# Kernel optimization log

Hardware: AMD Instinct MI355X
Metric: run time of the kernel (lower is better)

The kernel has to match this reference:

```python
import jax, jax.numpy as jnp
import numpy as np

B = 16384
MV = 512   # movie_vector_size
UV = 512   # user_vector_size
NM = 16    # num_dense_movie_embeddings
NU = 16    # num_dense_user_embeddings
DS = 16    # dense_embedding_size
MLP = [256, 128, 1]


def setup_inputs() -> dict:
    key = jax.random.key(0)
    ks = jax.random.split(key, 12)
    inp = {
        'movie_vectors': jax.random.normal(ks[0], (B, MV), jnp.float32),
        'user_vectors': jax.random.normal(ks[1], (B, UV), jnp.float32),
        # embedding towers: Linear(in, DS*N + 1), stored as [in, out]
        'Wm': jax.random.normal(ks[2], (MV, DS * NM + 1), jnp.float32) * (1.0 / np.sqrt(MV)),
        'bm': jax.random.normal(ks[3], (DS * NM + 1,), jnp.float32) * 0.01,
        'Wu': jax.random.normal(ks[4], (UV, DS * NU + 1), jnp.float32) * (1.0 / np.sqrt(UV)),
        'bu': jax.random.normal(ks[5], (DS * NU + 1,), jnp.float32) * 0.01,
    }
    d_in = (NM + NU) * DS  # 512
    dims = [d_in] + MLP
    for i in range(len(MLP)):
        inp[f'W{i+1}'] = jax.random.normal(ks[6 + 2*i], (dims[i], dims[i+1]), jnp.float32) * (1.0 / np.sqrt(dims[i]))
        inp[f'b{i+1}'] = jax.random.normal(ks[7 + 2*i], (dims[i+1],), jnp.float32) * 0.01
    return inp


def reference(movie_vectors, user_vectors, Wm, bm, Wu, bu, W1, b1, W2, b2, W3, b3):
    batch = movie_vectors.shape[0]
    movie_dense = movie_vectors @ Wm + bm          # [B, DS*NM+1]
    user_dense = user_vectors @ Wu + bu            # [B, DS*NU+1]
    fm_additive = movie_dense[:, -1] + user_dense[:, -1]            # [B]
    m_split = movie_dense[:, :-1].reshape(batch, NM, DS)            # [B, NM, DS]
    u_split = user_dense[:, :-1].reshape(batch, NU, DS)             # [B, NU, DS]
    fm_interactions = jnp.einsum('bik,bjk->bij', m_split, u_split).reshape(batch, -1)  # [B, NM*NU]
    all_dense = jnp.concatenate([movie_dense[:, :-1], user_dense[:, :-1]], axis=-1)    # [B, (NM+NU)*DS]
    h = jax.nn.relu(all_dense @ W1 + b1)
    h = jax.nn.relu(h @ W2 + b2)
    mlp_out = h @ W3 + b3                                           # [B, 1]
    logit = mlp_out + fm_additive[:, None] + jnp.sum(fm_interactions, axis=-1, keepdims=True)
    return logit
```

## Files before the change

### kernel.cpp

```cpp
#include <hip/hip_runtime.h>


#define NTH 1024
#define RB  64

typedef __bf16 bf16x8 __attribute__((ext_vector_type(8)));
typedef float  f32x4  __attribute__((ext_vector_type(4)));

#define WS_WMF  0
#define WS_WUF  294912
#define WS_W1F  589824
#define WS_W2F  851968
#define WS_BIAS 917504

#define BPITCH  528
#define L_BST   0
#define L_DENSE 67584
#define L_FM    133120
#define L_ADD   141824
#define L_OUT   142336
#define LDSB    142592

__device__ __forceinline__ unsigned short f2bf(float f) {
  unsigned u = __builtin_bit_cast(unsigned, f);
  u += 0x7FFFu + ((u >> 16) & 1u);
  return (unsigned short)(u >> 16);
}

__device__ __forceinline__ unsigned cvtpk(float a, float b) {
  unsigned r;
  asm("v_cvt_pk_bf16_f32 %0, %1, %2" : "=v"(r) : "v"(a), "v"(b));
  return r;
}

__device__ __forceinline__ f32x4 mfma_bf16(bf16x8 a, bf16x8 b, f32x4 c) {
  return __builtin_amdgcn_mfma_f32_16x16x32_bf16(a, b, c, 0, 0, 0);
}

extern "C" __global__ __launch_bounds__(256) void deepfm_prep(
    const float* __restrict__ Wm, const float* __restrict__ bm,
    const float* __restrict__ Wu, const float* __restrict__ bu,
    const float* __restrict__ W1, const float* __restrict__ W2,
    const float* __restrict__ b3, char* __restrict__ ws) {
  const int unit = blockIdx.x * 4 + (threadIdx.x >> 6);
  if (unit >= 897) return;
  const int l = threadIdx.x & 63;
  const int fi = l & 15, q = l >> 4;
  unsigned short h[8];
  if (unit < 576) {
    const int t = unit / 288, rem = unit % 288;
    const int kg = rem / 18, ft = rem % 18;
    const float* W = t ? Wu : Wm;
    char* outp = ws + (t ? WS_WUF : WS_WMF);
    const int f = ft * 16 + fi;
#pragma unroll
    for (int e = 0; e < 8; ++e) {
      const int k = kg * 32 + q * 8 + e;
      float val;
      if (f < 256) val = W[k * 257 + f];
      else if (f < 272) {
        float s = 0.f;
#pragma unroll
        for (int i = 0; i < 16; ++i) s += W[k * 257 + i * 16 + (f - 256)];
        val = s;
      } else if (f == 272) val = W[k * 257 + 256];
      else val = 0.f;
      h[e] = f2bf(val);
    }
    uint4 o;
    o.x = h[0] | ((unsigned)h[1] << 16); o.y = h[2] | ((unsigned)h[3] << 16);
    o.z = h[4] | ((unsigned)h[5] << 16); o.w = h[6] | ((unsigned)h[7] << 16);
    *(uint4*)(outp + (((kg * 18 + ft) * 64 + l) << 4)) = o;
  } else if (unit < 832) {
    const int bb = unit - 576;
    const int kg = bb / 16, ft = bb % 16;
    const int f = ft * 16 + fi;
#pragma unroll
    for (int e = 0; e < 8; ++e) h[e] = f2bf(W1[(kg * 32 + q * 8 + e) * 256 + f]);
    uint4 o;
    o.x = h[0] | ((unsigned)h[1] << 16); o.y = h[2] | ((unsigned)h[3] << 16);
    o.z = h[4] | ((unsigned)h[5] << 16); o.w = h[6] | ((unsigned)h[7] << 16);
    *(uint4*)(ws + WS_W1F + (((kg * 16 + ft) * 64 + l) << 4)) = o;
  } else if (unit < 896) {
    const int bb = unit - 832;
    const int kg = bb / 8, ft = bb % 8;
    const int f = ft * 16 + fi;
#pragma unroll
    for (int e = 0; e < 8; ++e) h[e] = f2bf(W2[(kg * 32 + q * 8 + e) * 128 + f]);
    uint4 o;
    o.x = h[0] | ((unsigned)h[1] << 16); o.y = h[2] | ((unsigned)h[3] << 16);
    o.z = h[4] | ((unsigned)h[5] << 16); o.w = h[6] | ((unsigned)h[7] << 16);
    *(uint4*)(ws + WS_W2F + (((kg * 8 + ft) * 64 + l) << 4)) = o;
  } else {
    float* aux = (float*)(ws + WS_BIAS);
    if (l < 16) {
      float s = 0.f;
      for (int i = 0; i < 16; ++i) s += bm[i * 16 + l];
      aux[l] = s;
    } else if (l < 32) {
      const int k = l - 16;
      float s = 0.f;
      for (int i = 0; i < 16; ++i) s += bu[i * 16 + k];
      aux[l] = s;
    } else if (l == 32) {
      aux[32] = bm[256] + bu[256] + b3[0];
    }
  }
}

extern "C" __global__ __launch_bounds__(NTH)
__attribute__((amdgpu_waves_per_eu(4, 4))) void deepfm_main(
    const float* __restrict__ movie, const float* __restrict__ user,
    const float* __restrict__ bm, const float* __restrict__ bu,
    const float* __restrict__ b1, const float* __restrict__ b2,
    const float* __restrict__ W3, const char* __restrict__ ws,
    float* __restrict__ out) {
  extern __shared__ __align__(16) char lds[];
  char* const bstage    = lds + L_BST;
  char* const densefrag = lds + L_DENSE;
  char* const h1frag    = lds + L_BST;
  float* const fmbuf    = (float*)(lds + L_FM);
  float* const addbuf   = (float*)(lds + L_ADD);
  float* const outpart  = (float*)(lds + L_OUT);

  const int tid = threadIdx.x;
  const int w   = tid >> 6;
  const int l   = tid & 63;
  const int cn  = l & 15;
  const int q   = l >> 4;
  const int row0 = blockIdx.x * RB;

  const int tw   = w >> 3;
  const int wi   = w & 7;
  const int axi  = wi & 1;
  const int rtb  = (wi >> 1) * 2;

  const int rot  = (int)blockIdx.x >> 3;
  const int hord = rot & 1;
  const int kk0  = (rot >> 1) & 7;
  const int p2r  = rot & 15;
  const int p3r  = rot & 7;

  const f32x4 zz = {0.f, 0.f, 0.f, 0.f};
  const float* auxb = (const float*)(ws + WS_BIAS);

  bf16x8 p2a, p2b;
  bf16x8 p3a, p3b;

  {
    const char* WF = ws + (tw ? WS_WUF : WS_WMF);
    const char* brow = bstage + tw * 64 * BPITCH;
    f32x4 a0r0 = zz, a0r1 = zz, a0r2 = zz, a0r3 = zz;
    f32x4 a1r0 = zz, a1r1 = zz, a1r2 = zz, a1r3 = zz;
    f32x4 axc0 = zz, axc1 = zz;

    const int h0 = hord, h1h = hord ^ 1;

#pragma unroll
    for (int p = 0; p < 8; ++p) {
      const int idx = p * 1024 + tid;
      const int rr = idx >> 6, f4 = idx & 63;
      const float* src = (rr >= 64) ? user : movie;
      const float4 v = *(const float4*)(src + (size_t)(row0 + (rr & 63)) * 512 +
                                        h0 * 256 + f4 * 4);
      uint2 o;
      o.x = cvtpk(v.x, v.y);
      o.y = cvtpk(v.z, v.w);
      *(uint2*)(bstage + rr * BPITCH + f4 * 8) = o;
    }
    __syncthreads();

    float4 pf[8];
#pragma unroll
    for (int p = 0; p < 8; ++p) {
      const int idx = p * 1024 + tid;
      const int rr = idx >> 6, f4 = idx & 63;
      const float* src = (rr >= 64) ? user : movie;
      pf[p] = *(const float4*)(src + (size_t)(row0 + (rr & 63)) * 512 +
                               h1h * 256 + f4 * 4);
    }
    uint2 pfc[8];

#pragma unroll
    for (int i = 0; i < 8; ++i) {
      const int kgl = (kk0 + i) & 7;
      const int kg  = h0 * 8 + kgl;
      const bf16x8 bf0 = *(const bf16x8*)(brow + cn * BPITCH + kgl * 64 + q * 16);
      const bf16x8 bf1 = *(const bf16x8*)(brow + (16 + cn) * BPITCH + kgl * 64 + q * 16);
      const bf16x8 bf2 = *(const bf16x8*)(brow + (32 + cn) * BPITCH + kgl * 64 + q * 16);
      const bf16x8 bf3 = *(const bf16x8*)(brow + (48 + cn) * BPITCH + kgl * 64 + q * 16);
      const bf16x8 A0 = *(const bf16x8*)(WF + (((kg * 18 + wi * 2 + 0) * 64 + l) << 4));
      const bf16x8 A1 = *(const bf16x8*)(WF + (((kg * 18 + wi * 2 + 1) * 64 + l) << 4));
      bf16x8 AX;
      if (wi < 4) AX = *(const bf16x8*)(WF + (((kg * 18 + 16 + axi) * 64 + l) << 4));
      __builtin_amdgcn_s_setprio(1);
      a0r0 = mfma_bf16(A0, bf0, a0r0);  a0r1 = mfma_bf16(A0, bf1, a0r1);
      a0r2 = mfma_bf16(A0, bf2, a0r2);  a0r3 = mfma_bf16(A0, bf3, a0r3);
      a1r0 = mfma_bf16(A1, bf0, a1r0);  a1r1 = mfma_bf16(A1, bf1, a1r1);
      a1r2 = mfma_bf16(A1, bf2, a1r2);  a1r3 = mfma_bf16(A1, bf3, a1r3);
      if (wi < 4) {
        const bf16x8 bs0 = rtb ? bf2 : bf0;
        const bf16x8 bs1 = rtb ? bf3 : bf1;
        axc0 = mfma_bf16(AX, bs0, axc0);
        axc1 = mfma_bf16(AX, bs1, axc1);
      }
      __builtin_amdgcn_s_setprio(0);
      if (i >= 1) {
        const int j = i - 1;
        pfc[j].x = cvtpk(pf[j].x, pf[j].y);
        pfc[j].y = cvtpk(pf[j].z, pf[j].w);
      }
    }
    pfc[7].x = cvtpk(pf[7].x, pf[7].y);
    pfc[7].y = cvtpk(pf[7].z, pf[7].w);

    __syncthreads();

    bf16x8 A0c = *(const bf16x8*)(WF + ((((h1h * 8 + kk0) * 18 + wi * 2 + 0) * 64 + l) << 4));
    bf16x8 A1c = *(const bf16x8*)(WF + ((((h1h * 8 + kk0) * 18 + wi * 2 + 1) * 64 + l) << 4));

#pragma unroll
    for (int p = 0; p < 8; ++p) {
      const int idx = p * 1024 + tid;
      const int rr = idx >> 6, f4 = idx & 63;
      *(uint2*)(bstage + rr * BPITCH + f4 * 8) = pfc[p];
    }
    __syncthreads();

#pragma unroll
    for (int i = 0; i < 8; ++i) {
      const int kgl = (kk0 + i) & 7;
      const int kg  = h1h * 8 + kgl;
      const bf16x8 bf0 = *(const bf16x8*)(brow + cn * BPITCH + kgl * 64 + q * 16);
      const bf16x8 bf1 = *(const bf16x8*)(brow + (16 + cn) * BPITCH + kgl * 64 + q * 16);
      const bf16x8 bf2 = *(const bf16x8*)(brow + (32 + cn) * BPITCH + kgl * 64 + q * 16);
      const bf16x8 bf3 = *(const bf16x8*)(brow + (48 + cn) * BPITCH + kgl * 64 + q * 16);
      bf16x8 AX;
      if (wi < 4) AX = *(const bf16x8*)(WF + (((kg * 18 + 16 + axi) * 64 + l) << 4));
      bf16x8 A0n, A1n;
      if (i < 7) {
        const int nkg = h1h * 8 + ((kk0 + i + 1) & 7);
        A0n = *(const bf16x8*)(WF + (((nkg * 18 + wi * 2 + 0) * 64 + l) << 4));
        A1n = *(const bf16x8*)(WF + (((nkg * 18 + wi * 2 + 1) * 64 + l) << 4));
      } else {
        A0n = A0c; A1n = A1c;
      }
      __builtin_amdgcn_s_setprio(1);
      a0r0 = mfma_bf16(A0c, bf0, a0r0);  a0r1 = mfma_bf16(A0c, bf1, a0r1);
      a0r2 = mfma_bf16(A0c, bf2, a0r2);  a0r3 = mfma_bf16(A0c, bf3, a0r3);
      a1r0 = mfma_bf16(A1c, bf0, a1r0);  a1r1 = mfma_bf16(A1c, bf1, a1r1);
      a1r2 = mfma_bf16(A1c, bf2, a1r2);  a1r3 = mfma_bf16(A1c, bf3, a1r3);
      if (wi < 4) {
        const bf16x8 bs0 = rtb ? bf2 : bf0;
        const bf16x8 bs1 = rtb ? bf3 : bf1;
        axc0 = mfma_bf16(AX, bs0, axc0);
        axc1 = mfma_bf16(AX, bs1, axc1);
      }
      __builtin_amdgcn_s_setprio(0);
      A0c = A0n; A1c = A1n;
    }

    p2a = *(const bf16x8*)(ws + WS_W1F + (((p2r * 16 + w) * 64 + l) << 4));
    p2b = *(const bf16x8*)(ws + WS_W1F + (((((p2r + 1) & 15) * 16 + w) * 64 + l) << 4));

    const float* bt = tw ? bu : bm;
    const f32x4 accA[2][4] = {{a0r0, a0r1, a0r2, a0r3}, {a1r0, a1r1, a1r2, a1r3}};
#pragma unroll
    for (int s = 0; s < 2; ++s) {
      const int ft = wi * 2 + s;
      const int fb = ft * 16 + q * 4;
      const float g0 = bt[fb], g1 = bt[fb + 1], g2 = bt[fb + 2], g3 = bt[fb + 3];
      const int kd = tw * 256 + fb;
      const int kgd = kd >> 5, qd = (kd >> 3) & 3, ed = kd & 4;
#pragma unroll
      for (int rt = 0; rt < 4; ++rt) {
        const f32x4 v = accA[s][rt];
        uint2 p;
        p.x = cvtpk(v[0] + g0, v[1] + g1);
        p.y = cvtpk(v[2] + g2, v[3] + g3);
        *(uint2*)(densefrag + (((kgd * 4 + rt) * 64 + qd * 16 + cn) << 4) +
                  (ed ? 8 : 0)) = p;
      }
    }

    if (wi < 4) {
      if (axi == 0) {
#pragma unroll
        for (int reg = 0; reg < 4; ++reg) {
          fmbuf[(tw * 64 + rtb * 16 + cn) * 17 + (q * 4 + reg)] = axc0[reg];
          fmbuf[(tw * 64 + (rtb + 1) * 16 + cn) * 17 + (q * 4 + reg)] = axc1[reg];
        }
      } else if (q == 0) {
        addbuf[tw * 64 + rtb * 16 + cn] = axc0[0];
        addbuf[tw * 64 + (rtb + 1) * 16 + cn] = axc1[0];
      }
    }
  }

  __syncthreads();

  if (tid < 64) {
    float p = 0.f;
#pragma unroll
    for (int k = 0; k < 16; ++k)
      p += (fmbuf[tid * 17 + k] + auxb[k]) *
           (fmbuf[(64 + tid) * 17 + k] + auxb[16 + k]);
    outpart[tid] = p + addbuf[tid] + addbuf[64 + tid] + auxb[32];
  }

  {
    const char* W1F = ws + WS_W1F;
    bf16x8 a0c = p2a;
    bf16x8 a0n = p2b;
    f32x4 r0 = zz, r1 = zz, r2 = zz, r3 = zz;
#pragma unroll
    for (int i = 0; i < 16; ++i) {
      const int kg = (p2r + i) & 15;
      const bf16x8 b0 = *(const bf16x8*)(densefrag + (((kg * 4 + 0) * 64 + l) << 4));
      const bf16x8 b1f = *(const bf16x8*)(densefrag + (((kg * 4 + 1) * 64 + l) << 4));
      const bf16x8 b2f = *(const bf16x8*)(densefrag + (((kg * 4 + 2) * 64 + l) << 4));
      const bf16x8 b3f = *(const bf16x8*)(densefrag + (((kg * 4 + 3) * 64 + l) << 4));
      bf16x8 a2;
      if (i < 14) {
        const int nkg = (p2r + i + 2) & 15;
        a2 = *(const bf16x8*)(W1F + (((nkg * 16 + w) * 64 + l) << 4));
      }
      __builtin_amdgcn_s_setprio(1);
      r0 = mfma_bf16(a0c, b0,  r0);
      r1 = mfma_bf16(a0c, b1f, r1);
      r2 = mfma_bf16(a0c, b2f, r2);
      r3 = mfma_bf16(a0c, b3f, r3);
      __builtin_amdgcn_s_setprio(0);
      a0c = a0n;
      if (i < 14) a0n = a2;
    }

    if (w < 8) {
      p3a = *(const bf16x8*)(ws + WS_W2F + (((p3r * 8 + w) * 64 + l) << 4));
      p3b = *(const bf16x8*)(ws + WS_W2F + (((((p3r + 1) & 7) * 8 + w) * 64 + l) << 4));
    }

    const f32x4 accA[4] = {r0, r1, r2, r3};
    const int fb = w * 16 + q * 4;
    const float g0 = b1[fb], g1 = b1[fb + 1], g2 = b1[fb + 2], g3 = b1[fb + 3];
    const int kgd = fb >> 5, qd = (fb >> 3) & 3, ed = fb & 4;
#pragma unroll
    for (int rt = 0; rt < 4; ++rt) {
      const f32x4 v = accA[rt];
      uint2 p;
      p.x = cvtpk(fmaxf(v[0] + g0, 0.f), fmaxf(v[1] + g1, 0.f));
      p.y = cvtpk(fmaxf(v[2] + g2, 0.f), fmaxf(v[3] + g3, 0.f));
      *(uint2*)(h1frag + (((kgd * 4 + rt) * 64 + qd * 16 + cn) << 4) +
                (ed ? 8 : 0)) = p;
    }
  }

  __syncthreads();

  if (w < 8) {
    const char* W2F = ws + WS_W2F;
    bf16x8 a0c = p3a;
    bf16x8 a0n = p3b;
    f32x4 d0 = zz, d1 = zz, d2 = zz, d3 = zz;
#pragma unroll
    for (int i = 0; i < 8; ++i) {
      const int kg = (p3r + i) & 7;
      const bf16x8 b0 = *(const bf16x8*)(h1frag + (((kg * 4 + 0) * 64 + l) << 4));
      const bf16x8 b1f = *(const bf16x8*)(h1frag + (((kg * 4 + 1) * 64 + l) << 4));
      const bf16x8 b2f = *(const bf16x8*)(h1frag + (((kg * 4 + 2) * 64 + l) << 4));
      const bf16x8 b3f = *(const bf16x8*)(h1frag + (((kg * 4 + 3) * 64 + l) << 4));
      bf16x8 a2;
      if (i < 6) {
        const int nkg = (p3r + i + 2) & 7;
        a2 = *(const bf16x8*)(W2F + (((nkg * 8 + w) * 64 + l) << 4));
      }
      d0 = mfma_bf16(a0c, b0,  d0);
      d1 = mfma_bf16(a0c, b1f, d1);
      d2 = mfma_bf16(a0c, b2f, d2);
      d3 = mfma_bf16(a0c, b3f, d3);
      a0c = a0n;
      if (i < 6) a0n = a2;
    }
    const int fb = w * 16 + q * 4;
    float bb[4], ww[4];
#pragma unroll
    for (int i = 0; i < 4; ++i) { bb[i] = b2[fb + i]; ww[i] = W3[fb + i]; }
    const f32x4 acc3[4] = {d0, d1, d2, d3};
#pragma unroll
    for (int j = 0; j < 4; ++j) {
      float p = 0.f;
#pragma unroll
      for (int reg = 0; reg < 4; ++reg)
        p += fmaxf(acc3[j][reg] + bb[reg], 0.f) * ww[reg];
      p += __shfl_xor(p, 16, 64);
      p += __shfl_xor(p, 32, 64);
      if (l < 16) atomicAdd(&outpart[j * 16 + cn], p);
    }
  }

  __syncthreads();
  if (tid < 64) out[row0 + tid] = outpart[tid];
}

extern "C" void kernel_launch(void* const* d_in, const int* in_sizes, int n_in,
                              void* d_out, int out_size, void* d_ws, size_t ws_size,
                              hipStream_t stream) {
  const float* movie = (const float*)d_in[0];
  const float* user  = (const float*)d_in[1];
  const float* Wm = (const float*)d_in[2];
  const float* bm = (const float*)d_in[3];
  const float* Wu = (const float*)d_in[4];
  const float* bu = (const float*)d_in[5];
  const float* W1 = (const float*)d_in[6];
  const float* b1 = (const float*)d_in[7];
  const float* W2 = (const float*)d_in[8];
  const float* b2 = (const float*)d_in[9];
  const float* W3 = (const float*)d_in[10];
  const float* b3 = (const float*)d_in[11];
  char* ws = (char*)d_ws;
  float* out = (float*)d_out;

  (void)hipFuncSetAttribute((const void*)deepfm_main,
                            hipFuncAttributeMaxDynamicSharedMemorySize, LDSB);

  deepfm_prep<<<225, 256, 0, stream>>>(Wm, bm, Wu, bu, W1, W2, b3, ws);
  deepfm_main<<<256, NTH, LDSB, stream>>>(movie, user, bm, bu, b1, b2, W3, ws, out);
}
```

Before: 129.5 us.

## Halve rows per block to 32 with 512 threads, doubling grid size

Result: no change. 132.0 us (+1.9%).

```diff
diff --git a/kernel.cpp b/kernel.cpp
--- a/kernel.cpp
+++ b/kernel.cpp
@@ -1,8 +1,9 @@
 #include <hip/hip_runtime.h>
 
 
-#define NTH 1024
-#define RB  64
+#define NTH 512
+#define RB  32
+#define NBLK 512
 
 typedef __bf16 bf16x8 __attribute__((ext_vector_type(8)));
 typedef float  f32x4  __attribute__((ext_vector_type(4)));
@@ -15,11 +16,11 @@
 
 #define BPITCH  528
 #define L_BST   0
-#define L_DENSE 67584
-#define L_FM    133120
-#define L_ADD   141824
-#define L_OUT   142336
-#define LDSB    142592
+#define L_DENSE 33792
+#define L_FM    66560
+#define L_ADD   70912
+#define L_OUT   71168
+#define LDSB    71296
 
 __device__ __forceinline__ unsigned short f2bf(float f) {
   unsigned u = __builtin_bit_cast(unsigned, f);
@@ -130,10 +131,10 @@
   const int q   = l >> 4;
   const int row0 = blockIdx.x * RB;
 
-  const int tw   = w >> 3;
-  const int wi   = w & 7;
+  const int tw   = w >> 2;
+  const int wi   = w & 3;
   const int axi  = wi & 1;
-  const int rtb  = (wi >> 1) * 2;
+  const int axrt = wi >> 1;
 
   const int rot  = (int)blockIdx.x >> 3;
   const int hord = rot & 1;
@@ -149,19 +150,18 @@
 
   {
     const char* WF = ws + (tw ? WS_WUF : WS_WMF);
-    const char* brow = bstage + tw * 64 * BPITCH;
-    f32x4 a0r0 = zz, a0r1 = zz, a0r2 = zz, a0r3 = zz;
-    f32x4 a1r0 = zz, a1r1 = zz, a1r2 = zz, a1r3 = zz;
-    f32x4 axc0 = zz, axc1 = zz;
+    const char* brow = bstage + tw * 32 * BPITCH;
+    f32x4 ar[4][2] = {{zz, zz}, {zz, zz}, {zz, zz}, {zz, zz}};
+    f32x4 axc = zz;
 
     const int h0 = hord, h1h = hord ^ 1;
 
 #pragma unroll
     for (int p = 0; p < 8; ++p) {
-      const int idx = p * 1024 + tid;
+      const int idx = p * NTH + tid;
       const int rr = idx >> 6, f4 = idx & 63;
-      const float* src = (rr >= 64) ? user : movie;
-      const float4 v = *(const float4*)(src + (size_t)(row0 + (rr & 63)) * 512 +
+      const float* src = (rr >= 32) ? user : movie;
+      const float4 v = *(const float4*)(src + (size_t)(row0 + (rr & 31)) * 512 +
                                         h0 * 256 + f4 * 4);
       uint2 o;
       o.x = cvtpk(v.x, v.y);
@@ -173,10 +173,10 @@
     float4 pf[8];
 #pragma unroll
     for (int p = 0; p < 8; ++p) {
-      const int idx = p * 1024 + tid;
+      const int idx = p * NTH + tid;
       const int rr = idx >> 6, f4 = idx & 63;
-      const float* src = (rr >= 64) ? user : movie;
-      pf[p] = *(const float4*)(src + (size_t)(row0 + (rr & 63)) * 512 +
+      const float* src = (rr >= 32) ? user : movie;
+      pf[p] = *(const float4*)(src + (size_t)(row0 + (rr & 31)) * 512 +
                                h1h * 256 + f4 * 4);
     }
     uint2 pfc[8];
@@ -187,23 +187,18 @@
       const int kg  = h0 * 8 + kgl;
       const bf16x8 bf0 = *(const bf16x8*)(brow + cn * BPITCH + kgl * 64 + q * 16);
       const bf16x8 bf1 = *(const bf16x8*)(brow + (16 + cn) * BPITCH + kgl * 64 + q * 16);
-      const bf16x8 bf2 = *(const bf16x8*)(brow + (32 + cn) * BPITCH + kgl * 64 + q * 16);
-      const bf16x8 bf3 = *(const bf16x8*)(brow + (48 + cn) * BPITCH + kgl * 64 + q * 16);
-      const bf16x8 A0 = *(const bf16x8*)(WF + (((kg * 18 + wi * 2 + 0) * 64 + l) << 4));
-      const bf16x8 A1 = *(const bf16x8*)(WF + (((kg * 18 + wi * 2 + 1) * 64 + l) << 4));
-      bf16x8 AX;
-      if (wi < 4) AX = *(const bf16x8*)(WF + (((kg * 18 + 16 + axi) * 64 + l) << 4));
+      bf16x8 A[4];
+#pragma unroll
+      for (int s = 0; s < 4; ++s)
+        A[s] = *(const bf16x8*)(WF + (((kg * 18 + wi * 4 + s) * 64 + l) << 4));
+      const bf16x8 AX = *(const bf16x8*)(WF + (((kg * 18 + 16 + axi) * 64 + l) << 4));
       __builtin_amdgcn_s_setprio(1);
-      a0r0 = mfma_bf16(A0, bf0, a0r0);  a0r1 = mfma_bf16(A0, bf1, a0r1);
-      a0r2 = mfma_bf16(A0, bf2, a0r2);  a0r3 = mfma_bf16(A0, bf3, a0r3);
-      a1r0 = mfma_bf16(A1, bf0, a1r0);  a1r1 = mfma_bf16(A1, bf1, a1r1);
-      a1r2 = mfma_bf16(A1, bf2, a1r2);  a1r3 = mfma_bf16(A1, bf3, a1r3);
-      if (wi < 4) {
-        const bf16x8 bs0 = rtb ? bf2 : bf0;
-        const bf16x8 bs1 = rtb ? bf3 : bf1;
-        axc0 = mfma_bf16(AX, bs0, axc0);
-        axc1 = mfma_bf16(AX, bs1, axc1);
-      }
+#pragma unroll
+      for (int s = 0; s < 4; ++s) {
+        ar[s][0] = mfma_bf16(A[s], bf0, ar[s][0]);
+        ar[s][1] = mfma_bf16(A[s], bf1, ar[s][1]);
+      }
+      axc = mfma_bf16(AX, axrt ? bf1 : bf0, axc);
       __builtin_amdgcn_s_setprio(0);
       if (i >= 1) {
         const int j = i - 1;
@@ -216,12 +211,14 @@
 
     __syncthreads();
 
-    bf16x8 A0c = *(const bf16x8*)(WF + ((((h1h * 8 + kk0) * 18 + wi * 2 + 0) * 64 + l) << 4));
-    bf16x8 A1c = *(const bf16x8*)(WF + ((((h1h * 8 + kk0) * 18 + wi * 2 + 1) * 64 + l) << 4));
+    bf16x8 Ac[4];
+#pragma unroll
+    for (int s = 0; s < 4; ++s)
+      Ac[s] = *(const bf16x8*)(WF + ((((h1h * 8 + kk0) * 18 + wi * 4 + s) * 64 + l) << 4));
 
 #pragma unroll
     for (int p = 0; p < 8; ++p) {
-      const int idx = p * 1024 + tid;
+      const int idx = p * NTH + tid;
       const int rr = idx >> 6, f4 = idx & 63;
       *(uint2*)(bstage + rr * BPITCH + f4 * 8) = pfc[p];
     }
@@ -233,142 +230,128 @@
       const int kg  = h1h * 8 + kgl;
       const bf16x8 bf0 = *(const bf16x8*)(brow + cn * BPITCH + kgl * 64 + q * 16);
       const bf16x8 bf1 = *(const bf16x8*)(brow + (16 + cn) * BPITCH + kgl * 64 + q * 16);
-      const bf16x8 bf2 = *(const bf16x8*)(brow + (32 + cn) * BPITCH + kgl * 64 + q * 16);
-      const bf16x8 bf3 = *(const bf16x8*)(brow + (48 + cn) * BPITCH + kgl * 64 + q * 16);
-      bf16x8 AX;
-      if (wi < 4) AX = *(const bf16x8*)(WF + (((kg * 18 + 16 + axi) * 64 + l) << 4));
-      bf16x8 A0n, A1n;
+      const bf16x8 AX = *(const bf16x8*)(WF + (((kg * 18 + 16 + axi) * 64 + l) << 4));
+      bf16x8 An[4];
       if (i < 7) {
         const int nkg = h1h * 8 + ((kk0 + i + 1) & 7);
-        A0n = *(const bf16x8*)(WF + (((nkg * 18 + wi * 2 + 0) * 64 + l) << 4));
-        A1n = *(const bf16x8*)(WF + (((nkg * 18 + wi * 2 + 1) * 64 + l) << 4));
+#pragma unroll
+        for (int s = 0; s < 4; ++s)
+          An[s] = *(const bf16x8*)(WF + (((nkg * 18 + wi * 4 + s) * 64 + l) << 4));
       } else {
-        A0n = A0c; A1n = A1c;
+#pragma unroll
+        for (int s = 0; s < 4; ++s) An[s] = Ac[s];
       }
       __builtin_amdgcn_s_setprio(1);
-      a0r0 = mfma_bf16(A0c, bf0, a0r0);  a0r1 = mfma_bf16(A0c, bf1, a0r1);
-      a0r2 = mfma_bf16(A0c, bf2, a0r2);  a0r3 = mfma_bf16(A0c, bf3, a0r3);
-      a1r0 = mfma_bf16(A1c, bf0, a1r0);  a1r1 = mfma_bf16(A1c, bf1, a1r1);
-      a1r2 = mfma_bf16(A1c, bf2, a1r2);  a1r3 = mfma_bf16(A1c, bf3, a1r3);
-      if (wi < 4) {
-        const bf16x8 bs0 = rtb ? bf2 : bf0;
-        const bf16x8 bs1 = rtb ? bf3 : bf1;
-        axc0 = mfma_bf16(AX, bs0, axc0);
-        axc1 = mfma_bf16(AX, bs1, axc1);
-      }
+#pragma unroll
+      for (int s = 0; s < 4; ++s) {
+        ar[s][0] = mfma_bf16(Ac[s], bf0, ar[s][0]);
+        ar[s][1] = mfma_bf16(Ac[s], bf1, ar[s][1]);
+      }
+      axc = mfma_bf16(AX, axrt ? bf1 : bf0, axc);
       __builtin_amdgcn_s_setprio(0);
-      A0c = A0n; A1c = A1n;
-    }
-
-    p2a = *(const bf16x8*)(ws + WS_W1F + (((p2r * 16 + w) * 64 + l) << 4));
-    p2b = *(const bf16x8*)(ws + WS_W1F + (((((p2r + 1) & 15) * 16 + w) * 64 + l) << 4));
+#pragma unroll
+      for (int s = 0; s < 4; ++s) Ac[s] = An[s];
+    }
+
+    p2a = *(const bf16x8*)(ws + WS_W1F + (((p2r * 16 + w * 2 + 0) * 64 + l) << 4));
+    p2b = *(const bf16x8*)(ws + WS_W1F + (((p2r * 16 + w * 2 + 1) * 64 + l) << 4));
 
     const float* bt = tw ? bu : bm;
-    const f32x4 accA[2][4] = {{a0r0, a0r1, a0r2, a0r3}, {a1r0, a1r1, a1r2, a1r3}};
-#pragma unroll
-    for (int s = 0; s < 2; ++s) {
-      const int ft = wi * 2 + s;
+#pragma unroll
+    for (int s = 0; s < 4; ++s) {
+      const int ft = wi * 4 + s;
       const int fb = ft * 16 + q * 4;
       const float g0 = bt[fb], g1 = bt[fb + 1], g2 = bt[fb + 2], g3 = bt[fb + 3];
       const int kd = tw * 256 + fb;
       const int kgd = kd >> 5, qd = (kd >> 3) & 3, ed = kd & 4;
 #pragma unroll
-      for (int rt = 0; rt < 4; ++rt) {
-        const f32x4 v = accA[s][rt];
+      for (int rt = 0; rt < 2; ++rt) {
+        const f32x4 v = ar[s][rt];
         uint2 p;
         p.x = cvtpk(v[0] + g0, v[1] + g1);
         p.y = cvtpk(v[2] + g2, v[3] + g3);
-        *(uint2*)(densefrag + (((kgd * 4 + rt) * 64 + qd * 16 + cn) << 4) +
+        *(uint2*)(densefrag + (((kgd * 2 + rt) * 64 + qd * 16 + cn) << 4) +
                   (ed ? 8 : 0)) = p;
       }
     }
 
-    if (wi < 4) {
-      if (axi == 0) {
-#pragma unroll
-        for (int reg = 0; reg < 4; ++reg) {
-          fmbuf[(tw * 64 + rtb * 16 + cn) * 17 + (q * 4 + reg)] = axc0[reg];
-          fmbuf[(tw * 64 + (rtb + 1) * 16 + cn) * 17 + (q * 4 + reg)] = axc1[reg];
-        }
-      } else if (q == 0) {
-        addbuf[tw * 64 + rtb * 16 + cn] = axc0[0];
-        addbuf[tw * 64 + (rtb + 1) * 16 + cn] = axc1[0];
-      }
+    if (axi == 0) {
+#pragma unroll
+      for (int reg = 0; reg < 4; ++reg)
+        fmbuf[(tw * 32 + axrt * 16 + cn) * 17 + (q * 4 + reg)] = axc[reg];
+    } else if (q == 0) {
+      addbuf[tw * 32 + axrt * 16 + cn] = axc[0];
     }
   }
 
   __syncthreads();
 
-  if (tid < 64) {
+  if (tid < 32) {
     float p = 0.f;
 #pragma unroll
     for (int k = 0; k < 16; ++k)
       p += (fmbuf[tid * 17 + k] + auxb[k]) *
-           (fmbuf[(64 + tid) * 17 + k] + auxb[16 + k]);
-    outpart[tid] = p + addbuf[tid] + addbuf[64 + tid] + auxb[32];
+           (fmbuf[(32 + tid) * 17 + k] + auxb[16 + k]);
+    outpart[tid] = p + addbuf[tid] + addbuf[32 + tid] + auxb[32];
   }
 
   {
     const char* W1F = ws + WS_W1F;
-    bf16x8 a0c = p2a;
-    bf16x8 a0n = p2b;
-    f32x4 r0 = zz, r1 = zz, r2 = zz, r3 = zz;
+    bf16x8 a0c = p2a, a1c = p2b;
+    f32x4 r[2][2] = {{zz, zz}, {zz, zz}};
 #pragma unroll
     for (int i = 0; i < 16; ++i) {
       const int kg = (p2r + i) & 15;
-      const bf16x8 b0 = *(const bf16x8*)(densefrag + (((kg * 4 + 0) * 64 + l) << 4));
-      const bf16x8 b1f = *(const bf16x8*)(densefrag + (((kg * 4 + 1) * 64 + l) << 4));
-      const bf16x8 b2f = *(const bf16x8*)(densefrag + (((kg * 4 + 2) * 64 + l) << 4));
-      const bf16x8 b3f = *(const bf16x8*)(densefrag + (((kg * 4 + 3) * 64 + l) << 4));
-      bf16x8 a2;
-      if (i < 14) {
-        const int nkg = (p2r + i + 2) & 15;
-        a2 = *(const bf16x8*)(W1F + (((nkg * 16 + w) * 64 + l) << 4));
+      const bf16x8 b0 = *(const bf16x8*)(densefrag + (((kg * 2 + 0) * 64 + l) << 4));
+      const bf16x8 b1f = *(const bf16x8*)(densefrag + (((kg * 2 + 1) * 64 + l) << 4));
+      bf16x8 a0n, a1n;
+      if (i < 15) {
+        const int nkg = (p2r + i + 1) & 15;
+        a0n = *(const bf16x8*)(W1F + (((nkg * 16 + w * 2 + 0) * 64 + l) << 4));
+        a1n = *(const bf16x8*)(W1F + (((nkg * 16 + w * 2 + 1) * 64 + l) << 4));
+      } else {
+        a0n = a0c; a1n = a1c;
       }
       __builtin_amdgcn_s_setprio(1);
-      r0 = mfma_bf16(a0c, b0,  r0);
-      r1 = mfma_bf16(a0c, b1f, r1);
-      r2 = mfma_bf16(a0c, b2f, r2);
-      r3 = mfma_bf16(a0c, b3f, r3);
+      r[0][0] = mfma_bf16(a0c, b0,  r[0][0]);
+      r[0][1] = mfma_bf16(a0c, b1f, r[0][1]);
+      r[1][0] = mfma_bf16(a1c, b0,  r[1][0]);
+      r[1][1] = mfma_bf16(a1c, b1f, r[1][1]);
       __builtin_amdgcn_s_setprio(0);
-      a0c = a0n;
-      if (i < 14) a0n = a2;
-    }
-
-    if (w < 8) {
-      p3a = *(const bf16x8*)(ws + WS_W2F + (((p3r * 8 + w) * 64 + l) << 4));
-      p3b = *(const bf16x8*)(ws + WS_W2F + (((((p3r + 1) & 7) * 8 + w) * 64 + l) << 4));
-    }
-
-    const f32x4 accA[4] = {r0, r1, r2, r3};
-    const int fb = w * 16 + q * 4;
-    const float g0 = b1[fb], g1 = b1[fb + 1], g2 = b1[fb + 2], g3 = b1[fb + 3];
-    const int kgd = fb >> 5, qd = (fb >> 3) & 3, ed = fb & 4;
-#pragma unroll
-    for (int rt = 0; rt < 4; ++rt) {
-      const f32x4 v = accA[rt];
-      uint2 p;
-      p.x = cvtpk(fmaxf(v[0] + g0, 0.f), fmaxf(v[1] + g1, 0.f));
-      p.y = cvtpk(fmaxf(v[2] + g2, 0.f), fmaxf(v[3] + g3, 0.f));
-      *(uint2*)(h1frag + (((kgd * 4 + rt) * 64 + qd * 16 + cn) << 4) +
-                (ed ? 8 : 0)) = p;
+      a0c = a0n; a1c = a1n;
+    }
+
+    p3a = *(const bf16x8*)(ws + WS_W2F + (((p3r * 8 + w) * 64 + l) << 4));
+    p3b = *(const bf16x8*)(ws + WS_W2F + (((((p3r + 1) & 7) * 8 + w) * 64 + l) << 4));
+
+#pragma unroll
+    for (int s = 0; s < 2; ++s) {
+      const int fb = (w * 2 + s) * 16 + q * 4;
+      const float g0 = b1[fb], g1 = b1[fb + 1], g2 = b1[fb + 2], g3 = b1[fb + 3];
+      const int kgd = fb >> 5, qd = (fb >> 3) & 3, ed = fb & 4;
+#pragma unroll
+      for (int rt = 0; rt < 2; ++rt) {
+        const f32x4 v = r[s][rt];
+        uint2 p;
+        p.x = cvtpk(fmaxf(v[0] + g0, 0.f), fmaxf(v[1] + g1, 0.f));
+        p.y = cvtpk(fmaxf(v[2] + g2, 0.f), fmaxf(v[3] + g3, 0.f));
+        *(uint2*)(h1frag + (((kgd * 2 + rt) * 64 + qd * 16 + cn) << 4) +
+                  (ed ? 8 : 0)) = p;
+      }
     }
   }
 
   __syncthreads();
 
-  if (w < 8) {
+  {
     const char* W2F = ws + WS_W2F;
-    bf16x8 a0c = p3a;
-    bf16x8 a0n = p3b;
-    f32x4 d0 = zz, d1 = zz, d2 = zz, d3 = zz;
+    bf16x8 a0c = p3a, a0n = p3b;
+    f32x4 d0 = zz, d1 = zz;
 #pragma unroll
     for (int i = 0; i < 8; ++i) {
       const int kg = (p3r + i) & 7;
-      const bf16x8 b0 = *(const bf16x8*)(h1frag + (((kg * 4 + 0) * 64 + l) << 4));
-      const bf16x8 b1f = *(const bf16x8*)(h1frag + (((kg * 4 + 1) * 64 + l) << 4));
-      const bf16x8 b2f = *(const bf16x8*)(h1frag + (((kg * 4 + 2) * 64 + l) << 4));
-      const bf16x8 b3f = *(const bf16x8*)(h1frag + (((kg * 4 + 3) * 64 + l) << 4));
+      const bf16x8 b0 = *(const bf16x8*)(h1frag + (((kg * 2 + 0) * 64 + l) << 4));
+      const bf16x8 b1f = *(const bf16x8*)(h1frag + (((kg * 2 + 1) * 64 + l) << 4));
       bf16x8 a2;
       if (i < 6) {
         const int nkg = (p3r + i + 2) & 7;
@@ -376,8 +359,6 @@
       }
       d0 = mfma_bf16(a0c, b0,  d0);
       d1 = mfma_bf16(a0c, b1f, d1);
-      d2 = mfma_bf16(a0c, b2f, d2);
-      d3 = mfma_bf16(a0c, b3f, d3);
       a0c = a0n;
       if (i < 6) a0n = a2;
     }
@@ -385,9 +366,9 @@
     float bb[4], ww[4];
 #pragma unroll
     for (int i = 0; i < 4; ++i) { bb[i] = b2[fb + i]; ww[i] = W3[fb + i]; }
-    const f32x4 acc3[4] = {d0, d1, d2, d3};
-#pragma unroll
-    for (int j = 0; j < 4; ++j) {
+    const f32x4 acc3[2] = {d0, d1};
+#pragma unroll
+    for (int j = 0; j < 2; ++j) {
       float p = 0.f;
 #pragma unroll
       for (int reg = 0; reg < 4; ++reg)
@@ -399,7 +380,7 @@
   }
 
   __syncthreads();
-  if (tid < 64) out[row0 + tid] = outpart[tid];
+  if (tid < 32) out[row0 + tid] = outpart[tid];
 }
 
 extern "C" void kernel_launch(void* const* d_in, const int* in_sizes, int n_in,
@@ -424,5 +405,5 @@
                             hipFuncAttributeMaxDynamicSharedMemorySize, LDSB);
 
   deepfm_prep<<<225, 256, 0, stream>>>(Wm, bm, Wu, bu, W1, W2, b3, ws);
-  deepfm_main<<<256, NTH, LDSB, stream>>>(movie, user, bm, bu, b1, b2, W3, ws, out);
-}
+  deepfm_main<<<NBLK, NTH, LDSB, stream>>>(movie, user, bm, bu, b1, b2, W3, ws, out);
+}
```

## Stage full K input tile at once and drop two-half prefetch pipeline

Applied to the files above, without the earlier changes.

New measurement: 130.9 us. About the same (+1.1%).

```diff
diff --git a/kernel.cpp b/kernel.cpp
--- a/kernel.cpp
+++ b/kernel.cpp
@@ -13,13 +13,14 @@
 #define WS_W2F  851968
 #define WS_BIAS 917504
 
-#define BPITCH  528
+#define BPITCH  1040
 #define L_BST   0
-#define L_DENSE 67584
-#define L_FM    133120
-#define L_ADD   141824
-#define L_OUT   142336
-#define LDSB    142592
+#define L_DENSE 0
+#define L_H1    65536
+#define L_FM    98304
+#define L_ADD   107008
+#define L_OUT   107520
+#define LDSB    133120
 
 __device__ __forceinline__ unsigned short f2bf(float f) {
   unsigned u = __builtin_bit_cast(unsigned, f);
@@ -118,7 +119,7 @@
   extern __shared__ __align__(16) char lds[];
   char* const bstage    = lds + L_BST;
   char* const densefrag = lds + L_DENSE;
-  char* const h1frag    = lds + L_BST;
+  char* const h1frag    = lds + L_H1;
   float* const fmbuf    = (float*)(lds + L_FM);
   float* const addbuf   = (float*)(lds + L_ADD);
   float* const outpart  = (float*)(lds + L_OUT);
@@ -136,8 +137,7 @@
   const int rtb  = (wi >> 1) * 2;
 
   const int rot  = (int)blockIdx.x >> 3;
-  const int hord = rot & 1;
-  const int kk0  = (rot >> 1) & 7;
+  const int kk0  = rot & 15;
   const int p2r  = rot & 15;
   const int p3r  = rot & 7;
 
@@ -154,15 +154,16 @@
     f32x4 a1r0 = zz, a1r1 = zz, a1r2 = zz, a1r3 = zz;
     f32x4 axc0 = zz, axc1 = zz;
 
-    const int h0 = hord, h1h = hord ^ 1;
-
-#pragma unroll
-    for (int p = 0; p < 8; ++p) {
+    bf16x8 A0c = *(const bf16x8*)(WF + (((kk0 * 18 + wi * 2 + 0) * 64 + l) << 4));
+    bf16x8 A1c = *(const bf16x8*)(WF + (((kk0 * 18 + wi * 2 + 1) * 64 + l) << 4));
+
+#pragma unroll
+    for (int p = 0; p < 16; ++p) {
       const int idx = p * 1024 + tid;
-      const int rr = idx >> 6, f4 = idx & 63;
+      const int rr = idx >> 7, f4 = idx & 127;
       const float* src = (rr >= 64) ? user : movie;
       const float4 v = *(const float4*)(src + (size_t)(row0 + (rr & 63)) * 512 +
-                                        h0 * 256 + f4 * 4);
+                                        f4 * 4);
       uint2 o;
       o.x = cvtpk(v.x, v.y);
       o.y = cvtpk(v.z, v.w);
@@ -170,76 +171,18 @@
     }
     __syncthreads();
 
-    float4 pf[8];
-#pragma unroll
-    for (int p = 0; p < 8; ++p) {
-      const int idx = p * 1024 + tid;
-      const int rr = idx >> 6, f4 = idx & 63;
-      const float* src = (rr >= 64) ? user : movie;
-      pf[p] = *(const float4*)(src + (size_t)(row0 + (rr & 63)) * 512 +
-                               h1h * 256 + f4 * 4);
-    }
-    uint2 pfc[8];
-
-#pragma unroll
-    for (int i = 0; i < 8; ++i) {
-      const int kgl = (kk0 + i) & 7;
-      const int kg  = h0 * 8 + kgl;
-      const bf16x8 bf0 = *(const bf16x8*)(brow + cn * BPITCH + kgl * 64 + q * 16);
-      const bf16x8 bf1 = *(const bf16x8*)(brow + (16 + cn) * BPITCH + kgl * 64 + q * 16);
-      const bf16x8 bf2 = *(const bf16x8*)(brow + (32 + cn) * BPITCH + kgl * 64 + q * 16);
-      const bf16x8 bf3 = *(const bf16x8*)(brow + (48 + cn) * BPITCH + kgl * 64 + q * 16);
-      const bf16x8 A0 = *(const bf16x8*)(WF + (((kg * 18 + wi * 2 + 0) * 64 + l) << 4));
-      const bf16x8 A1 = *(const bf16x8*)(WF + (((kg * 18 + wi * 2 + 1) * 64 + l) << 4));
-      bf16x8 AX;
-      if (wi < 4) AX = *(const bf16x8*)(WF + (((kg * 18 + 16 + axi) * 64 + l) << 4));
-      __builtin_amdgcn_s_setprio(1);
-      a0r0 = mfma_bf16(A0, bf0, a0r0);  a0r1 = mfma_bf16(A0, bf1, a0r1);
-      a0r2 = mfma_bf16(A0, bf2, a0r2);  a0r3 = mfma_bf16(A0, bf3, a0r3);
-      a1r0 = mfma_bf16(A1, bf0, a1r0);  a1r1 = mfma_bf16(A1, bf1, a1r1);
-      a1r2 = mfma_bf16(A1, bf2, a1r2);  a1r3 = mfma_bf16(A1, bf3, a1r3);
-      if (wi < 4) {
-        const bf16x8 bs0 = rtb ? bf2 : bf0;
-        const bf16x8 bs1 = rtb ? bf3 : bf1;
-        axc0 = mfma_bf16(AX, bs0, axc0);
-        axc1 = mfma_bf16(AX, bs1, axc1);
-      }
-      __builtin_amdgcn_s_setprio(0);
-      if (i >= 1) {
-        const int j = i - 1;
-        pfc[j].x = cvtpk(pf[j].x, pf[j].y);
-        pfc[j].y = cvtpk(pf[j].z, pf[j].w);
-      }
-    }
-    pfc[7].x = cvtpk(pf[7].x, pf[7].y);
-    pfc[7].y = cvtpk(pf[7].z, pf[7].w);
-
-    __syncthreads();
-
-    bf16x8 A0c = *(const bf16x8*)(WF + ((((h1h * 8 + kk0) * 18 + wi * 2 + 0) * 64 + l) << 4));
-    bf16x8 A1c = *(const bf16x8*)(WF + ((((h1h * 8 + kk0) * 18 + wi * 2 + 1) * 64 + l) << 4));
-
-#pragma unroll
-    for (int p = 0; p < 8; ++p) {
-      const int idx = p * 1024 + tid;
-      const int rr = idx >> 6, f4 = idx & 63;
-      *(uint2*)(bstage + rr * BPITCH + f4 * 8) = pfc[p];
-    }
-    __syncthreads();
-
-#pragma unroll
-    for (int i = 0; i < 8; ++i) {
-      const int kgl = (kk0 + i) & 7;
-      const int kg  = h1h * 8 + kgl;
-      const bf16x8 bf0 = *(const bf16x8*)(brow + cn * BPITCH + kgl * 64 + q * 16);
-      const bf16x8 bf1 = *(const bf16x8*)(brow + (16 + cn) * BPITCH + kgl * 64 + q * 16);
-      const bf16x8 bf2 = *(const bf16x8*)(brow + (32 + cn) * BPITCH + kgl * 64 + q * 16);
-      const bf16x8 bf3 = *(const bf16x8*)(brow + (48 + cn) * BPITCH + kgl * 64 + q * 16);
+#pragma unroll
+    for (int i = 0; i < 16; ++i) {
+      const int kg = (kk0 + i) & 15;
+      const bf16x8 bf0 = *(const bf16x8*)(brow + cn * BPITCH + kg * 64 + q * 16);
+      const bf16x8 bf1 = *(const bf16x8*)(brow + (16 + cn) * BPITCH + kg * 64 + q * 16);
+      const bf16x8 bf2 = *(const bf16x8*)(brow + (32 + cn) * BPITCH + kg * 64 + q * 16);
+      const bf16x8 bf3 = *(const bf16x8*)(brow + (48 + cn) * BPITCH + kg * 64 + q * 16);
       bf16x8 AX;
       if (wi < 4) AX = *(const bf16x8*)(WF + (((kg * 18 + 16 + axi) * 64 + l) << 4));
       bf16x8 A0n, A1n;
-      if (i < 7) {
-        const int nkg = h1h * 8 + ((kk0 + i + 1) & 7);
+      if (i < 15) {
+        const int nkg = (kk0 + i + 1) & 15;
         A0n = *(const bf16x8*)(WF + (((nkg * 18 + wi * 2 + 0) * 64 + l) << 4));
         A1n = *(const bf16x8*)(WF + (((nkg * 18 + wi * 2 + 1) * 64 + l) << 4));
       } else {
@@ -262,6 +205,8 @@
 
     p2a = *(const bf16x8*)(ws + WS_W1F + (((p2r * 16 + w) * 64 + l) << 4));
     p2b = *(const bf16x8*)(ws + WS_W1F + (((((p2r + 1) & 15) * 16 + w) * 64 + l) << 4));
+
+    __syncthreads();
 
     const float* bt = tw ? bu : bm;
     const f32x4 accA[2][4] = {{a0r0, a0r1, a0r2, a0r3}, {a1r0, a1r1, a1r2, a1r3}};
```
